# Performance work log

Hardware: AMD Instinct MI355X
Metric: run time of the kernel (lower is better)

Reference implementation:

```python
import jax, jax.numpy as jnp
import numpy as np

B, S, D, H = 8, 1024, 768, 16
PD = D // H  # projection dims per head


def setup_inputs() -> dict:
    key = jax.random.key(0)
    ks = jax.random.split(key, 9)
    s = 1.0 / np.sqrt(D)
    return {
        "inputs": jax.random.normal(ks[0], (B, S, D), dtype=jnp.float32),
        "Wq": jax.random.normal(ks[1], (D, D), dtype=jnp.float32) * s,
        "bq": jnp.zeros((D,), dtype=jnp.float32),
        "Wk": jax.random.normal(ks[2], (D, D), dtype=jnp.float32) * s,
        "bk": jnp.zeros((D,), dtype=jnp.float32),
        "Wv": jax.random.normal(ks[3], (D, D), dtype=jnp.float32) * s,
        "bv": jnp.zeros((D,), dtype=jnp.float32),
        "Wo": jax.random.normal(ks[4], (D, D), dtype=jnp.float32) * s,
        "bo": jnp.zeros((D,), dtype=jnp.float32),
    }


def _split_heads(x):
    # [B,S,D] -> [B,H,S,PD]
    return x.reshape(B, S, H, PD).transpose(0, 2, 1, 3)


def reference(inputs, Wq, bq, Wk, bk, Wv, bv, Wo, bo):
    q = _split_heads(inputs @ Wq + bq)
    k = _split_heads(inputs @ Wk + bk)
    v = _split_heads(inputs @ Wv + bv)
    scale = 1.0 / jnp.sqrt(jnp.asarray(PD, dtype=q.dtype))
    scores = jnp.einsum("bhqd,bhkd->bhqk", q, k) * scale
    weights = jax.nn.softmax(scores, axis=-1)
    attn = jnp.einsum("bhqk,bhkd->bhqd", weights, v)
    concat = attn.transpose(0, 2, 1, 3).reshape(B, S, D)
    return concat @ Wo + bo
```

## Files before the change

### kernel.cpp

```cpp
#include <hip/hip_runtime.h>
#include <hip/hip_bf16.h>

#define B_   8
#define S_   1024
#define D_   768
#define H_   16
#define PD_  48
#define PDP  64
#define M_   8192
#define BH_  128

#define QSCALE 0.20823031f

typedef __attribute__((ext_vector_type(8))) short short8;
typedef __attribute__((ext_vector_type(4))) float floatx4;

__device__ __forceinline__ unsigned short f2bf(float f) {
    __hip_bfloat16 h = __float2bfloat16(f);
    return *reinterpret_cast<unsigned short*>(&h);
}

__device__ __forceinline__ void async_copy16(const unsigned short* gptr, unsigned short* lptr) {
    __builtin_amdgcn_global_load_lds(
        (const __attribute__((address_space(1))) unsigned int*)gptr,
        (__attribute__((address_space(3))) unsigned int*)lptr, 16, 0, 0);
}

__global__ __launch_bounds__(256) void prep_kernel(
    const float* __restrict__ X, unsigned short* __restrict__ Xb,
    const float* __restrict__ w0, const float* __restrict__ w1,
    const float* __restrict__ w2, const float* __restrict__ w3,
    unsigned short* __restrict__ Wtall) {
    __shared__ float tile[32][33];
    const int tid = threadIdx.x;
    const int bx = blockIdx.x;
    if (bx < 6144) {
        long i = ((long)bx * 256 + tid) * 4;
        float4 v = *(const float4*)(X + i);
        ushort4 o;
        o.x = f2bf(v.x); o.y = f2bf(v.y); o.z = f2bf(v.z); o.w = f2bf(v.w);
        *(ushort4*)(Xb + i) = o;
        return;
    }
    const int t = bx - 6144;
    const int z = t / 576, r = t % 576;
    const int nt = (r % 24) * 32, kt = (r / 24) * 32;
    const int tx = tid & 31, ty = tid >> 5;
    const float* W = (z == 0) ? w0 : (z == 1) ? w1 : (z == 2) ? w2 : w3;
    unsigned short* Wt = Wtall + (long)z * D_ * D_;
#pragma unroll
    for (int i = 0; i < 4; i++)
        tile[ty + i * 8][tx] = W[(long)(kt + ty + i * 8) * D_ + nt + tx];
    __syncthreads();
#pragma unroll
    for (int i = 0; i < 4; i++)
        Wt[(long)(nt + ty + i * 8) * D_ + kt + tx] = f2bf(tile[tx][ty + i * 8]);
}

__device__ __forceinline__ void gemm_core(
    const unsigned short* __restrict__ Ag,
    const unsigned short* __restrict__ Btg,
    unsigned short* Asm, unsigned short* Bsm, floatx4 acc[4][4]) {
    const int tid = threadIdx.x;
    const int lane = tid & 63, w = tid >> 6;
    const int wr = (w >> 1) * 64, wc = (w & 1) * 64;
    const int l15 = lane & 15, l4 = lane >> 4;
    const floatx4 zero = {0.f, 0.f, 0.f, 0.f};
#pragma unroll
    for (int mt = 0; mt < 4; mt++)
#pragma unroll
        for (int nt = 0; nt < 4; nt++) acc[mt][nt] = zero;

    for (int kb = 0; kb < D_; kb += 64) {
#pragma unroll
        for (int i = 0; i < 4; i++) {
            int c = tid + i * 256;
            int row = c >> 3, seg = (c & 7) ^ (row & 7);
            long goff = (long)row * D_ + kb + seg * 8;
            async_copy16(&Ag[goff], &Asm[c * 8]);
            async_copy16(&Btg[goff], &Bsm[c * 8]);
        }
        __syncthreads();
#pragma unroll
        for (int kk = 0; kk < 2; kk++) {
            short8 af[4], bf[4];
#pragma unroll
            for (int mt = 0; mt < 4; mt++) {
                int r = wr + mt * 16 + l15;
                af[mt] = *(const short8*)&Asm[r * 64 + (((kk * 4 + l4) ^ (r & 7)) * 8)];
            }
#pragma unroll
            for (int nt = 0; nt < 4; nt++) {
                int c = wc + nt * 16 + l15;
                bf[nt] = *(const short8*)&Bsm[c * 64 + (((kk * 4 + l4) ^ (c & 7)) * 8)];
            }
#pragma unroll
            for (int mt = 0; mt < 4; mt++)
#pragma unroll
                for (int nt = 0; nt < 4; nt++)
                    acc[mt][nt] = __builtin_amdgcn_mfma_f32_16x16x32_bf16(
                        af[mt], bf[nt], acc[mt][nt], 0, 0, 0);
        }
        __syncthreads();
    }
}

__global__ __launch_bounds__(256) void gemm_qkv_kernel(
    const unsigned short* __restrict__ Xb, const unsigned short* __restrict__ Wtall,
    const float* __restrict__ bq, const float* __restrict__ bk,
    const float* __restrict__ bv, unsigned short* __restrict__ QKV) {
    __shared__ __align__(16) unsigned short Asm[128 * 64];
    __shared__ __align__(16) unsigned short Bsm[128 * 64];
    const int z = blockIdx.z;
    const int m0 = blockIdx.x * 128, n0 = blockIdx.y * 128;
    const float* bias = (z == 0) ? bq : (z == 1) ? bk : bv;
    const float vscale = (z == 0) ? QSCALE : 1.0f;
    floatx4 acc[4][4];
    gemm_core(Xb + (long)m0 * D_, Wtall + (long)z * D_ * D_ + (long)n0 * D_, Asm, Bsm, acc);

    unsigned short* out = QKV + (long)z * BH_ * S_ * PDP;
    const int tid = threadIdx.x, lane = tid & 63, w = tid >> 6;
    const int wr = (w >> 1) * 64, wc = (w & 1) * 64;
    const int l15 = lane & 15, l4 = lane >> 4;
#pragma unroll
    for (int nt = 0; nt < 4; nt++) {
        int n = n0 + wc + nt * 16 + l15;
        int h = n / PD_, pd = n % PD_;
        float bb = bias[n];
#pragma unroll
        for (int mt = 0; mt < 4; mt++) {
#pragma unroll
            for (int r = 0; r < 4; r++) {
                int m = m0 + wr + mt * 16 + l4 * 4 + r;
                int b = m >> 10, s = m & 1023;
                out[((long)(b * H_ + h) * S_ + s) * PDP + pd] = f2bf((acc[mt][nt][r] + bb) * vscale);
            }
        }
    }
}

__global__ __launch_bounds__(256) void transpose_v_kernel(
    const unsigned short* __restrict__ V, unsigned short* __restrict__ Vt) {
    __shared__ __align__(16) unsigned short T[64 * 64];
    const int tid = threadIdx.x;
    const int st = blockIdx.x * 64, bh = blockIdx.y;
    const unsigned short* src = V + (long)bh * S_ * PDP;
    unsigned short* dst = Vt + (long)bh * PDP * S_;
#pragma unroll
    for (int i = 0; i < 2; i++) {
        int c = tid + i * 256;
        int row = c >> 3, seg = (c & 7) ^ (row & 7);
        async_copy16(&src[(long)(st + row) * PDP + seg * 8], &T[c * 8]);
    }
    __syncthreads();
    const int d = tid >> 2;
    unsigned short tmp[16];
#pragma unroll
    for (int j = 0; j < 16; j++) {
        int sl = (tid & 3) * 16 + j;
        unsigned short v = T[sl * 64 + ((d >> 3) ^ (sl & 7)) * 8 + (d & 7)];
        tmp[j] = (d < PD_) ? v : ((d == PD_) ? (unsigned short)0x3F80 : (unsigned short)0);
    }
    *(uint4*)&dst[(long)d * S_ + st + (tid & 3) * 16] = *(uint4*)&tmp[0];
    *(uint4*)&dst[(long)d * S_ + st + (tid & 3) * 16 + 8] = *(uint4*)&tmp[8];
}

__global__ __launch_bounds__(256) void gemm_out_kernel(
    const unsigned short* __restrict__ Ctx, const unsigned short* __restrict__ Wot,
    const float* __restrict__ bo, float* __restrict__ Out) {
    __shared__ __align__(16) unsigned short Asm[128 * 64];
    __shared__ __align__(16) unsigned short Bsm[128 * 64];
    const int m0 = blockIdx.x * 128, n0 = blockIdx.y * 128;
    floatx4 acc[4][4];
    gemm_core(Ctx + (long)m0 * D_, Wot + (long)n0 * D_, Asm, Bsm, acc);

    const int tid = threadIdx.x, lane = tid & 63, w = tid >> 6;
    const int wr = (w >> 1) * 64, wc = (w & 1) * 64;
    const int l15 = lane & 15, l4 = lane >> 4;
#pragma unroll
    for (int nt = 0; nt < 4; nt++) {
        int n = n0 + wc + nt * 16 + l15;
        float bb = bo[n];
#pragma unroll
        for (int mt = 0; mt < 4; mt++) {
#pragma unroll
            for (int r = 0; r < 4; r++) {
                int m = m0 + wr + mt * 16 + l4 * 4 + r;
                Out[(long)m * D_ + n] = acc[mt][nt][r] + bb;
            }
        }
    }
}

__global__ __launch_bounds__(256) void attn_kernel(
    const unsigned short* __restrict__ Qg, const unsigned short* __restrict__ Kg,
    const unsigned short* __restrict__ Vtg, unsigned short* __restrict__ Ctx) {
    __shared__ __align__(16) unsigned short Ks[64 * 64];
    __shared__ __align__(16) unsigned short Vs[64 * 64];
    __shared__ __align__(16) unsigned short Ps[4][64 * 64];
    const int tid = threadIdx.x, lane = tid & 63, w = tid >> 6;
    const int l15 = lane & 15, l4 = lane >> 4;
    const int bh = blockIdx.x, qt = blockIdx.y;
    const long qkbase = (long)bh * S_ * PDP;
    const long vbase  = (long)bh * PDP * S_;

    short8 bq[4][2];
#pragma unroll
    for (int g = 0; g < 4; g++) {
        int qrow = qt * 256 + w * 64 + g * 16 + l15;
        bq[g][0] = *(const short8*)&Qg[qkbase + (long)qrow * PDP + l4 * 8];
        bq[g][1] = *(const short8*)&Qg[qkbase + (long)qrow * PDP + 32 + l4 * 8];
    }
    if (l4 >= 2) {
        const short8 z8 = {0, 0, 0, 0, 0, 0, 0, 0};
#pragma unroll
        for (int g = 0; g < 4; g++) bq[g][1] = z8;
    }

    const floatx4 zero = {0.f, 0.f, 0.f, 0.f};
    floatx4 accO[4][4];
#pragma unroll
    for (int g = 0; g < 4; g++)
#pragma unroll
        for (int nt = 0; nt < 4; nt++) accO[g][nt] = zero;

    unsigned short* Pw = &Ps[w][0];

    for (int kt = 0; kt < 16; kt++) {
        __syncthreads();
#pragma unroll
        for (int i = 0; i < 2; i++) {
            int c = tid + i * 256;
            int row = c >> 3, seg = (c & 7) ^ (row & 7);
            async_copy16(&Kg[qkbase + (long)(kt * 64 + row) * PDP + seg * 8], &Ks[c * 8]);
            async_copy16(&Vtg[vbase + (long)row * S_ + kt * 64 + seg * 8], &Vs[c * 8]);
        }
        __syncthreads();

        short8 ak[4][2];
#pragma unroll
        for (int ks = 0; ks < 4; ks++) {
            int kr = ks * 16 + l15;
            ak[ks][0] = *(const short8*)&Ks[kr * 64 + ((l4 ^ (kr & 7)) * 8)];
            ak[ks][1] = *(const short8*)&Ks[kr * 64 + (((4 + l4) ^ (kr & 7)) * 8)];
        }

#pragma unroll
        for (int g = 0; g < 4; g++) {
            floatx4 sc[4];
#pragma unroll
            for (int ks = 0; ks < 4; ks++) {
                floatx4 a = zero;
                a = __builtin_amdgcn_mfma_f32_16x16x32_bf16(ak[ks][0], bq[g][0], a, 0, 0, 0);
                a = __builtin_amdgcn_mfma_f32_16x16x32_bf16(ak[ks][1], bq[g][1], a, 0, 0, 0);
                sc[ks] = a;
            }
            int prow = g * 16 + l15;
#pragma unroll
            for (int ks = 0; ks < 4; ks++) {
                unsigned short p4[4];
#pragma unroll
                for (int r = 0; r < 4; r++) p4[r] = f2bf(__builtin_amdgcn_exp2f(sc[ks][r]));
                int addr = prow * 64 + (((ks * 2 + (l4 >> 1)) ^ (prow & 7)) * 8) + (l4 & 1) * 4;
                *(uint2*)&Pw[addr] = *(uint2*)&p4[0];
            }
        }

#pragma unroll
        for (int kk = 0; kk < 2; kk++) {
            short8 bv[4];
#pragma unroll
            for (int nt = 0; nt < 4; nt++) {
                int vr = nt * 16 + l15;
                bv[nt] = *(const short8*)&Vs[vr * 64 + (((kk * 4 + l4) ^ (vr & 7)) * 8)];
            }
#pragma unroll
            for (int g = 0; g < 4; g++) {
                int prow = g * 16 + l15;
                short8 ap = *(const short8*)&Pw[prow * 64 + (((kk * 4 + l4) ^ (prow & 7)) * 8)];
#pragma unroll
                for (int nt = 0; nt < 4; nt++)
                    accO[g][nt] = __builtin_amdgcn_mfma_f32_16x16x32_bf16(ap, bv[nt], accO[g][nt], 0, 0, 0);
            }
        }
    }

    const int b = bh >> 4, h = bh & 15;
#pragma unroll
    for (int g = 0; g < 4; g++) {
#pragma unroll
        for (int r = 0; r < 4; r++) {
            float lsum = __shfl(accO[g][3][r], lane & 48);
            float inv = 1.0f / lsum;
            int q = qt * 256 + w * 64 + g * 16 + l4 * 4 + r;
            long rowoff = (long)(b * S_ + q) * D_ + h * PD_;
#pragma unroll
            for (int nt = 0; nt < 3; nt++)
                Ctx[rowoff + nt * 16 + l15] = f2bf(accO[g][nt][r] * inv);
        }
    }
}

extern "C" void kernel_launch(void* const* d_in, const int* in_sizes, int n_in,
                              void* d_out, int out_size, void* d_ws, size_t ws_size,
                              hipStream_t stream) {
    const float* X  = (const float*)d_in[0];
    const float* Wq = (const float*)d_in[1];
    const float* bq = (const float*)d_in[2];
    const float* Wk = (const float*)d_in[3];
    const float* bk = (const float*)d_in[4];
    const float* Wv = (const float*)d_in[5];
    const float* bv = (const float*)d_in[6];
    const float* Wo = (const float*)d_in[7];
    const float* bo = (const float*)d_in[8];

    unsigned char* ws = (unsigned char*)d_ws;
    const long XB_BYTES  = (long)M_ * D_ * 2;
    const long WT_BYTES  = (long)D_ * D_ * 2;
    const long QKV_BYTES = (long)BH_ * S_ * PDP * 2;

    unsigned short* Xbf   = (unsigned short*)(ws);
    unsigned short* Wtall = (unsigned short*)(ws + XB_BYTES);
    unsigned short* Qws   = (unsigned short*)(ws + XB_BYTES + 4 * WT_BYTES);
    unsigned short* Kws   = Qws + QKV_BYTES / 2;
    unsigned short* Vws   = Kws + QKV_BYTES / 2;
    unsigned short* Vtws  = Vws + QKV_BYTES / 2;
    unsigned short* Ctx   = Vws;

    prep_kernel<<<8448, 256, 0, stream>>>(X, Xbf, Wq, Wk, Wv, Wo, Wtall);
    gemm_qkv_kernel<<<dim3(64, 6, 3), 256, 0, stream>>>(Xbf, Wtall, bq, bk, bv, Qws);
    transpose_v_kernel<<<dim3(16, 128), 256, 0, stream>>>(Vws, Vtws);
    attn_kernel<<<dim3(128, 4), 256, 0, stream>>>(Qws, Kws, Vtws, Ctx);
    gemm_out_kernel<<<dim3(64, 6), 256, 0, stream>>>(
        Ctx, Wtall + 3 * (WT_BYTES / 2), bo, (float*)d_out);
}
```

Baseline: 195.9 us.

## Fuse V transpose into QKV GEMM epilogue and use cheaper bf16 packing

The QKV GEMM now writes V straight into the transposed [bh, d, s] layout, packing bf16 pairs, and writes the row of ones used for the softmax denominator. This lets the separate transpose_v kernel and its extra read/write pass over V be removed. The bf16 conversion is replaced by an add-and-shift round (round-half-up, no NaN or RNE handling) with perm-based pair packing, used in prep, the epilogue and the attention P writes. Pad rows 49-63 of Vt are no longer zero-filled, so they rely on those columns being ignored downstream. Ctx now gets its own buffer instead of aliasing V.

```diff
diff --git a/kernel.cpp b/kernel.cpp
--- a/kernel.cpp
+++ b/kernel.cpp
@@ -16,8 +16,12 @@
 typedef __attribute__((ext_vector_type(4))) float floatx4;
 
 __device__ __forceinline__ unsigned short f2bf(float f) {
-    __hip_bfloat16 h = __float2bfloat16(f);
-    return *reinterpret_cast<unsigned short*>(&h);
+    return (unsigned short)((__float_as_uint(f) + 0x8000u) >> 16);
+}
+__device__ __forceinline__ unsigned int pack_bf2(float lo, float hi) {
+    unsigned a = __float_as_uint(hi) + 0x8000u;
+    unsigned b = __float_as_uint(lo) + 0x8000u;
+    return __builtin_amdgcn_perm(a, b, 0x07060302u);
 }
 
 __device__ __forceinline__ void async_copy16(const unsigned short* gptr, unsigned short* lptr) {
@@ -37,9 +41,10 @@
     if (bx < 6144) {
         long i = ((long)bx * 256 + tid) * 4;
         float4 v = *(const float4*)(X + i);
-        ushort4 o;
-        o.x = f2bf(v.x); o.y = f2bf(v.y); o.z = f2bf(v.z); o.w = f2bf(v.w);
-        *(ushort4*)(Xb + i) = o;
+        uint2 o;
+        o.x = pack_bf2(v.x, v.y);
+        o.y = pack_bf2(v.z, v.w);
+        *(uint2*)(Xb + i) = o;
         return;
     }
     const int t = bx - 6144;
@@ -108,7 +113,8 @@
 __global__ __launch_bounds__(256) void gemm_qkv_kernel(
     const unsigned short* __restrict__ Xb, const unsigned short* __restrict__ Wtall,
     const float* __restrict__ bq, const float* __restrict__ bk,
-    const float* __restrict__ bv, unsigned short* __restrict__ QKV) {
+    const float* __restrict__ bv, unsigned short* __restrict__ QK,
+    unsigned short* __restrict__ Vt) {
     __shared__ __align__(16) unsigned short Asm[128 * 64];
     __shared__ __align__(16) unsigned short Bsm[128 * 64];
     const int z = blockIdx.z;
@@ -118,10 +124,39 @@
     floatx4 acc[4][4];
     gemm_core(Xb + (long)m0 * D_, Wtall + (long)z * D_ * D_ + (long)n0 * D_, Asm, Bsm, acc);
 
-    unsigned short* out = QKV + (long)z * BH_ * S_ * PDP;
     const int tid = threadIdx.x, lane = tid & 63, w = tid >> 6;
     const int wr = (w >> 1) * 64, wc = (w & 1) * 64;
     const int l15 = lane & 15, l4 = lane >> 4;
+    const int b = m0 >> 10, sbase = m0 & 1023;
+
+    if (z == 2) {
+#pragma unroll
+        for (int nt = 0; nt < 4; nt++) {
+            int n = n0 + wc + nt * 16 + l15;
+            int h = n / PD_, pd = n % PD_;
+            float bb = bias[n];
+            long rowbase = ((long)(b * H_ + h) * PDP + pd) * S_;
+#pragma unroll
+            for (int mt = 0; mt < 4; mt++) {
+                uint2 pp;
+                pp.x = pack_bf2(acc[mt][nt][0] + bb, acc[mt][nt][1] + bb);
+                pp.y = pack_bf2(acc[mt][nt][2] + bb, acc[mt][nt][3] + bb);
+                int s = sbase + wr + mt * 16 + l4 * 4;
+                *(uint2*)&Vt[rowbase + s] = pp;
+            }
+        }
+        const int h0 = n0 / PD_, h1 = (n0 + 127) / PD_;
+        if (tid < 32) {
+            const uint2 ones = {0x3F803F80u, 0x3F803F80u};
+            for (int h = h0; h <= h1; h++) {
+                long off = ((long)(b * H_ + h) * PDP + PD_) * S_ + sbase + tid * 4;
+                *(uint2*)&Vt[off] = ones;
+            }
+        }
+        return;
+    }
+
+    unsigned short* out = QK + (long)z * BH_ * S_ * PDP;
 #pragma unroll
     for (int nt = 0; nt < 4; nt++) {
         int n = n0 + wc + nt * 16 + l15;
@@ -131,38 +166,11 @@
         for (int mt = 0; mt < 4; mt++) {
 #pragma unroll
             for (int r = 0; r < 4; r++) {
-                int m = m0 + wr + mt * 16 + l4 * 4 + r;
-                int b = m >> 10, s = m & 1023;
+                int s = sbase + wr + mt * 16 + l4 * 4 + r;
                 out[((long)(b * H_ + h) * S_ + s) * PDP + pd] = f2bf((acc[mt][nt][r] + bb) * vscale);
             }
         }
     }
-}
-
-__global__ __launch_bounds__(256) void transpose_v_kernel(
-    const unsigned short* __restrict__ V, unsigned short* __restrict__ Vt) {
-    __shared__ __align__(16) unsigned short T[64 * 64];
-    const int tid = threadIdx.x;
-    const int st = blockIdx.x * 64, bh = blockIdx.y;
-    const unsigned short* src = V + (long)bh * S_ * PDP;
-    unsigned short* dst = Vt + (long)bh * PDP * S_;
-#pragma unroll
-    for (int i = 0; i < 2; i++) {
-        int c = tid + i * 256;
-        int row = c >> 3, seg = (c & 7) ^ (row & 7);
-        async_copy16(&src[(long)(st + row) * PDP + seg * 8], &T[c * 8]);
-    }
-    __syncthreads();
-    const int d = tid >> 2;
-    unsigned short tmp[16];
-#pragma unroll
-    for (int j = 0; j < 16; j++) {
-        int sl = (tid & 3) * 16 + j;
-        unsigned short v = T[sl * 64 + ((d >> 3) ^ (sl & 7)) * 8 + (d & 7)];
-        tmp[j] = (d < PD_) ? v : ((d == PD_) ? (unsigned short)0x3F80 : (unsigned short)0);
-    }
-    *(uint4*)&dst[(long)d * S_ + st + (tid & 3) * 16] = *(uint4*)&tmp[0];
-    *(uint4*)&dst[(long)d * S_ + st + (tid & 3) * 16 + 8] = *(uint4*)&tmp[8];
 }
 
 __global__ __launch_bounds__(256) void gemm_out_kernel(
@@ -258,11 +266,13 @@
             int prow = g * 16 + l15;
 #pragma unroll
             for (int ks = 0; ks < 4; ks++) {
-                unsigned short p4[4];
-#pragma unroll
-                for (int r = 0; r < 4; r++) p4[r] = f2bf(__builtin_amdgcn_exp2f(sc[ks][r]));
+                uint2 pp;
+                pp.x = pack_bf2(__builtin_amdgcn_exp2f(sc[ks][0]),
+                                __builtin_amdgcn_exp2f(sc[ks][1]));
+                pp.y = pack_bf2(__builtin_amdgcn_exp2f(sc[ks][2]),
+                                __builtin_amdgcn_exp2f(sc[ks][3]));
                 int addr = prow * 64 + (((ks * 2 + (l4 >> 1)) ^ (prow & 7)) * 8) + (l4 & 1) * 4;
-                *(uint2*)&Pw[addr] = *(uint2*)&p4[0];
+                *(uint2*)&Pw[addr] = pp;
             }
         }
 
@@ -321,16 +331,13 @@
 
     unsigned short* Xbf   = (unsigned short*)(ws);
     unsigned short* Wtall = (unsigned short*)(ws + XB_BYTES);
-    unsigned short* Qws   = (unsigned short*)(ws + XB_BYTES + 4 * WT_BYTES);
-    unsigned short* Kws   = Qws + QKV_BYTES / 2;
-    unsigned short* Vws   = Kws + QKV_BYTES / 2;
-    unsigned short* Vtws  = Vws + QKV_BYTES / 2;
-    unsigned short* Ctx   = Vws;
+    unsigned short* QKws  = (unsigned short*)(ws + XB_BYTES + 4 * WT_BYTES);
+    unsigned short* Vtws  = QKws + 2 * (QKV_BYTES / 2);
+    unsigned short* Ctx   = Vtws + QKV_BYTES / 2;
 
     prep_kernel<<<8448, 256, 0, stream>>>(X, Xbf, Wq, Wk, Wv, Wo, Wtall);
-    gemm_qkv_kernel<<<dim3(64, 6, 3), 256, 0, stream>>>(Xbf, Wtall, bq, bk, bv, Qws);
-    transpose_v_kernel<<<dim3(16, 128), 256, 0, stream>>>(Vws, Vtws);
-    attn_kernel<<<dim3(128, 4), 256, 0, stream>>>(Qws, Kws, Vtws, Ctx);
+    gemm_qkv_kernel<<<dim3(64, 6, 3), 256, 0, stream>>>(Xbf, Wtall, bq, bk, bv, QKws, Vtws);
+    attn_kernel<<<dim3(128, 4), 256, 0, stream>>>(QKws, QKws + QKV_BYTES / 2, Vtws, Ctx);
     gemm_out_kernel<<<dim3(64, 6), 256, 0, stream>>>(
         Ctx, Wtall + 3 * (WT_BYTES / 2), bo, (float*)d_out);
 }
```

New measurement: 206.6 us. +5.5%, slower.

## Load K/V fragments directly from global memory and use cheaper bf16 packing

Applied to the files above, without the earlier changes.

The attention kernel no longer stages K and V tiles through shared memory with async copies and two block barriers per iteration. Each wave now reads its MFMA operand fragments straight from global memory, which relies on L1/L2 reuse across the four waves. Float-to-bf16 conversion switches to a round-half-up add-shift packed with a byte permute, replacing round-to-nearest-even and dropping NaN handling. The QKV epilogue also hoists the batch index out of the inner loop. The trade is fewer syncs and less LDS use against redundant global loads per wave and slightly different rounding.

```diff
diff --git a/kernel.cpp b/kernel.cpp
--- a/kernel.cpp
+++ b/kernel.cpp
@@ -16,8 +16,12 @@
 typedef __attribute__((ext_vector_type(4))) float floatx4;
 
 __device__ __forceinline__ unsigned short f2bf(float f) {
-    __hip_bfloat16 h = __float2bfloat16(f);
-    return *reinterpret_cast<unsigned short*>(&h);
+    return (unsigned short)((__float_as_uint(f) + 0x8000u) >> 16);
+}
+__device__ __forceinline__ unsigned int pack_bf2(float lo, float hi) {
+    unsigned a = __float_as_uint(hi) + 0x8000u;
+    unsigned b = __float_as_uint(lo) + 0x8000u;
+    return __builtin_amdgcn_perm(a, b, 0x07060302u);
 }
 
 __device__ __forceinline__ void async_copy16(const unsigned short* gptr, unsigned short* lptr) {
@@ -37,9 +41,10 @@
     if (bx < 6144) {
         long i = ((long)bx * 256 + tid) * 4;
         float4 v = *(const float4*)(X + i);
-        ushort4 o;
-        o.x = f2bf(v.x); o.y = f2bf(v.y); o.z = f2bf(v.z); o.w = f2bf(v.w);
-        *(ushort4*)(Xb + i) = o;
+        uint2 o;
+        o.x = pack_bf2(v.x, v.y);
+        o.y = pack_bf2(v.z, v.w);
+        *(uint2*)(Xb + i) = o;
         return;
     }
     const int t = bx - 6144;
@@ -122,6 +127,7 @@
     const int tid = threadIdx.x, lane = tid & 63, w = tid >> 6;
     const int wr = (w >> 1) * 64, wc = (w & 1) * 64;
     const int l15 = lane & 15, l4 = lane >> 4;
+    const int b = m0 >> 10, sbase = m0 & 1023;
 #pragma unroll
     for (int nt = 0; nt < 4; nt++) {
         int n = n0 + wc + nt * 16 + l15;
@@ -131,8 +137,7 @@
         for (int mt = 0; mt < 4; mt++) {
 #pragma unroll
             for (int r = 0; r < 4; r++) {
-                int m = m0 + wr + mt * 16 + l4 * 4 + r;
-                int b = m >> 10, s = m & 1023;
+                int s = sbase + wr + mt * 16 + l4 * 4 + r;
                 out[((long)(b * H_ + h) * S_ + s) * PDP + pd] = f2bf((acc[mt][nt][r] + bb) * vscale);
             }
         }
@@ -195,8 +200,6 @@
 __global__ __launch_bounds__(256) void attn_kernel(
     const unsigned short* __restrict__ Qg, const unsigned short* __restrict__ Kg,
     const unsigned short* __restrict__ Vtg, unsigned short* __restrict__ Ctx) {
-    __shared__ __align__(16) unsigned short Ks[64 * 64];
-    __shared__ __align__(16) unsigned short Vs[64 * 64];
     __shared__ __align__(16) unsigned short Ps[4][64 * 64];
     const int tid = threadIdx.x, lane = tid & 63, w = tid >> 6;
     const int l15 = lane & 15, l4 = lane >> 4;
@@ -227,22 +230,12 @@
     unsigned short* Pw = &Ps[w][0];
 
     for (int kt = 0; kt < 16; kt++) {
-        __syncthreads();
-#pragma unroll
-        for (int i = 0; i < 2; i++) {
-            int c = tid + i * 256;
-            int row = c >> 3, seg = (c & 7) ^ (row & 7);
-            async_copy16(&Kg[qkbase + (long)(kt * 64 + row) * PDP + seg * 8], &Ks[c * 8]);
-            async_copy16(&Vtg[vbase + (long)row * S_ + kt * 64 + seg * 8], &Vs[c * 8]);
-        }
-        __syncthreads();
-
         short8 ak[4][2];
 #pragma unroll
         for (int ks = 0; ks < 4; ks++) {
-            int kr = ks * 16 + l15;
-            ak[ks][0] = *(const short8*)&Ks[kr * 64 + ((l4 ^ (kr & 7)) * 8)];
-            ak[ks][1] = *(const short8*)&Ks[kr * 64 + (((4 + l4) ^ (kr & 7)) * 8)];
+            const unsigned short* kr = &Kg[qkbase + (long)(kt * 64 + ks * 16 + l15) * PDP];
+            ak[ks][0] = *(const short8*)&kr[l4 * 8];
+            ak[ks][1] = *(const short8*)&kr[32 + l4 * 8];
         }
 
 #pragma unroll
@@ -258,11 +251,13 @@
             int prow = g * 16 + l15;
 #pragma unroll
             for (int ks = 0; ks < 4; ks++) {
-                unsigned short p4[4];
-#pragma unroll
-                for (int r = 0; r < 4; r++) p4[r] = f2bf(__builtin_amdgcn_exp2f(sc[ks][r]));
+                uint2 pp;
+                pp.x = pack_bf2(__builtin_amdgcn_exp2f(sc[ks][0]),
+                                __builtin_amdgcn_exp2f(sc[ks][1]));
+                pp.y = pack_bf2(__builtin_amdgcn_exp2f(sc[ks][2]),
+                                __builtin_amdgcn_exp2f(sc[ks][3]));
                 int addr = prow * 64 + (((ks * 2 + (l4 >> 1)) ^ (prow & 7)) * 8) + (l4 & 1) * 4;
-                *(uint2*)&Pw[addr] = *(uint2*)&p4[0];
+                *(uint2*)&Pw[addr] = pp;
             }
         }
 
@@ -271,8 +266,8 @@
             short8 bv[4];
 #pragma unroll
             for (int nt = 0; nt < 4; nt++) {
-                int vr = nt * 16 + l15;
-                bv[nt] = *(const short8*)&Vs[vr * 64 + (((kk * 4 + l4) ^ (vr & 7)) * 8)];
+                int d = nt * 16 + l15;
+                bv[nt] = *(const short8*)&Vtg[vbase + (long)d * S_ + kt * 64 + kk * 32 + l4 * 8];
             }
 #pragma unroll
             for (int g = 0; g < 4; g++) {
```

Result: slower. 223.4 us (+14.0%).
